# Optimization experiments

Hardware: AMD Instinct MI355X
Metric: run time of the kernel (lower is better)

## Reference

```python
import jax, jax.numpy as jnp
import numpy as np

B, D, K, NUM_CLASSES = 8192, 512, 20, 1024
EPS = 1e-12  # torch F.normalize clamp


def setup_inputs() -> dict:
    key = jax.random.key(0)
    k1, k2 = jax.random.split(key)
    batch = jax.random.normal(k1, (B, D), dtype=jnp.float32)
    labels = jax.random.randint(k2, (B,), 0, NUM_CLASSES, dtype=jnp.int64 if jax.config.jax_enable_x64 else jnp.int32)
    return {"batch": batch, "labels": labels, "k": K}


def reference(batch, labels, k):
    # L2-normalize rows (F.normalize, p=2)
    norm = jnp.maximum(jnp.linalg.norm(batch, axis=1, keepdims=True), EPS)
    x = batch / norm
    cos = x @ x.T                                   # [B, B] cosine similarity
    min_value = cos.min() - 1.0                     # scalar, computed before diag fill
    bs = cos.shape[0]
    diag = jnp.eye(bs, dtype=bool)
    cos = jnp.where(diag, min_value, cos)           # fill_diagonal_(min_value)
    # argsort(-cos)[:, :k]  ==  top-k by similarity (self excluded via diag fill)
    top_vals, top_idx = jax.lax.top_k(cos, k)       # [B, k]
    # preds = (cos + 1)/2 gathered at neighbor indices == (top_vals + 1)/2
    preds = (top_vals + 1.0) * 0.5
    true_labels = (labels[top_idx] == labels[:, None]).astype(jnp.float32)  # [B, k]
    # nn.BCELoss with mean reduction; torch clamps each log term at -100
    logp = jnp.maximum(jnp.log(preds), -100.0)
    log1mp = jnp.maximum(jnp.log1p(-preds), -100.0)
    loss = -(true_labels * logp + (1.0 - true_labels) * log1mp)
    return loss.mean()
```

## Files before the change

### kernel.cpp

```cpp
#include <hip/hip_runtime.h>
#include <hip/hip_bf16.h>

#define NROWS 8192
#define DIM   512
#define KSEL  20
#define PANEL 1024
#define NSURV 512

typedef unsigned int u32;
typedef unsigned long long u64;
typedef short bf16x8 __attribute__((ext_vector_type(8)));
typedef float f32x4 __attribute__((ext_vector_type(4)));
typedef ushort u16x2 __attribute__((ext_vector_type(2)));

typedef const void __attribute__((address_space(1))) as1_void;
typedef void __attribute__((address_space(3))) as3_void;

__device__ __forceinline__ void async_ld16(const ushort* g, ushort* l) {
    __builtin_amdgcn_global_load_lds((as1_void*)g, (as3_void*)l, 16, 0, 0);
}

__device__ __forceinline__ ushort f2bf(float f) {
    u32 u = __float_as_uint(f);
    return (ushort)((u + 0x7FFFu + ((u >> 16) & 1u)) >> 16);
}

__device__ __forceinline__ u32 mono16(u32 r) {
    return r ^ (0x8000u | ((r >> 15) * 0x7FFFu));
}

__device__ __forceinline__ u32 mkey(float f) { return mono16((u32)f2bf(f)); }

__device__ __forceinline__ u32 pkmax(u32 a, u32 b) {
    union { u32 u; u16x2 v; } x, y; x.u = a; y.u = b;
    x.v = __builtin_elementwise_max(x.v, y.v);
    return x.u;
}

__global__ __launch_bounds__(256) void k_norm(const float* __restrict__ x,
                                              ushort* __restrict__ xn) {
    int lane = threadIdx.x & 63;
    int wv   = threadIdx.x >> 6;
    int row  = blockIdx.x * 4 + wv;
    const float4* xr = (const float4*)(x + (size_t)row * DIM);
    float4 a = xr[2 * lane];
    float4 b = xr[2 * lane + 1];
    float ss = a.x*a.x + a.y*a.y + a.z*a.z + a.w*a.w
             + b.x*b.x + b.y*b.y + b.z*b.z + b.w*b.w;
    #pragma unroll
    for (int off = 32; off; off >>= 1) ss += __shfl_xor(ss, off);
    float sc = 1.0f / fmaxf(sqrtf(ss), 1e-12f);
    float v[8] = {a.x*sc, a.y*sc, a.z*sc, a.w*sc, b.x*sc, b.y*sc, b.z*sc, b.w*sc};
    union { ushort u[8]; uint4 q; } o;
    #pragma unroll
    for (int i = 0; i < 8; ++i) o.u[i] = f2bf(v[i]);
    *(uint4*)(xn + (size_t)row * DIM + lane * 8) = o.q;
}

template<bool TRI>
__global__ __launch_bounds__(256) void k_gemm(const ushort* __restrict__ xn,
                                              ushort* __restrict__ C,
                                              ushort* __restrict__ M,
                                              int row0) {
    __shared__ ushort sh[128 * 128];
    ushort* lA = sh;
    ushort* lB = sh + 128 * 64;
    int tid  = threadIdx.x;
    int lane = tid & 63, wv = tid >> 6;
    int wr = wv >> 1, wc = wv & 1;
    int q = lane >> 4, m = lane & 15;
    int bx, by;
    if (TRI) {
        int t = (int)blockIdx.x;
        t = (t & 7) * 260 + (t >> 3);
        by = (int)((sqrtf(8.0f * (float)t + 1.0f) - 1.0f) * 0.5f);
        while ((by + 1) * (by + 2) / 2 <= t) ++by;
        while (by * (by + 1) / 2 > t) --by;
        bx = t - by * (by + 1) / 2;
    } else {
        bx = blockIdx.x; by = blockIdx.y;
    }
    int grow0 = row0 + by * 128;
    int gcol0 = bx * 128;
    f32x4 acc[4][4] = {};

    int lr = lane >> 3;
    int lc = lane & 7;
    for (int kc = 0; kc < 8; ++kc) {
        #pragma unroll
        for (int t = 0; t < 4; ++t) {
            int rb  = wv * 32 + t * 8;
            int r   = rb + lr;
            int fch = lc ^ (r & 7);
            async_ld16(xn + (size_t)(grow0 + r) * DIM + kc * 64 + fch * 8, &lA[rb * 64]);
            async_ld16(xn + (size_t)(gcol0 + r) * DIM + kc * 64 + fch * 8, &lB[rb * 64]);
        }
        __syncthreads();
        #pragma unroll
        for (int s = 0; s < 2; ++s) {
            bf16x8 af[4], bfr[4];
            #pragma unroll
            for (int i = 0; i < 4; ++i) {
                int ra = wr * 64 + i * 16 + m;
                af[i]  = *(const bf16x8*)&lA[ra * 64 + (((s * 4 + q) ^ (ra & 7)) * 8)];
                int rb2 = wc * 64 + i * 16 + m;
                bfr[i] = *(const bf16x8*)&lB[rb2 * 64 + (((s * 4 + q) ^ (rb2 & 7)) * 8)];
            }
            #pragma unroll
            for (int i = 0; i < 4; ++i)
                #pragma unroll
                for (int j = 0; j < 4; ++j)
                    acc[i][j] = __builtin_amdgcn_mfma_f32_16x16x32_bf16(af[i], bfr[j], acc[i][j], 0, 0, 0);
        }
        __syncthreads();
    }

    float cmf[4] = {-3.0f, -3.0f, -3.0f, -3.0f};
    #pragma unroll
    for (int i = 0; i < 4; ++i) {
        float rmf[4] = {-3.0f, -3.0f, -3.0f, -3.0f};
        int rloc = wr * 64 + i * 16 + q * 4;
        #pragma unroll
        for (int j = 0; j < 4; ++j) {
            int cl = wc * 64 + j * 16 + m;
            int c  = gcol0 + cl;
            #pragma unroll
            for (int reg = 0; reg < 4; ++reg) {
                int r    = rloc + reg;
                int grw  = row0 + by * 128 + r;
                float a  = acc[i][j][reg];
                bool dg  = (grw == c);
                float mv = dg ? -3.0f : a;
                rmf[reg] = fmaxf(rmf[reg], mv);
                cmf[j]   = fmaxf(cmf[j], mv);
                int D = r * 64 + ((cl >> 1) ^ (q << 3));
                sh[D * 2 + (cl & 1)] = dg ? (ushort)0xC040 : f2bf(a);
            }
        }
        u32 p01 = mkey(rmf[0]) | (mkey(rmf[1]) << 16);
        u32 p23 = mkey(rmf[2]) | (mkey(rmf[3]) << 16);
        #pragma unroll
        for (int off = 1; off <= 8; off <<= 1) {
            p01 = pkmax(p01, (u32)__shfl_xor((int)p01, off));
            p23 = pkmax(p23, (u32)__shfl_xor((int)p23, off));
        }
        if (m == 0) {
            u64 pk = (u64)p01 | ((u64)p23 << 32);
            *(u64*)&M[(size_t)(bx * 2 + wc) * NROWS + (row0 + by * 128 + rloc)] = pk;
        }
    }
    if (TRI && bx != by) {
        u32 q01 = mkey(cmf[0]) | (mkey(cmf[1]) << 16);
        u32 q23 = mkey(cmf[2]) | (mkey(cmf[3]) << 16);
        q01 = pkmax(q01, (u32)__shfl_xor((int)q01, 16));
        q01 = pkmax(q01, (u32)__shfl_xor((int)q01, 32));
        q23 = pkmax(q23, (u32)__shfl_xor((int)q23, 16));
        q23 = pkmax(q23, (u32)__shfl_xor((int)q23, 32));
        if (q == 0) {
            int gc = gcol0 + wc * 64 + m;
            size_t sb = (size_t)(by * 2 + wr) * NROWS + gc;
            M[sb +  0] = (ushort)(q01 & 0xFFFFu);
            M[sb + 16] = (ushort)(q01 >> 16);
            M[sb + 32] = (ushort)(q23 & 0xFFFFu);
            M[sb + 48] = (ushort)(q23 >> 16);
        }
    }
    __syncthreads();

    int tr = tid >> 4;
    int tc = tid & 15;
    #pragma unroll
    for (int p = 0; p < 8; ++p) {
        int r  = p * 16 + tr;
        int qr = (r >> 2) & 3;
        uint4 v = *(const uint4*)&sh[(r * 64 + ((tc * 4) ^ (qr << 3))) * 2];
        *(uint4*)&C[(size_t)(by * 128 + r) * NROWS + gcol0 + tc * 8] = v;
    }

    if (TRI && bx != by) {
        __syncthreads();
        u32* sh32 = (u32*)sh;
        #pragma unroll
        for (int i = 0; i < 4; ++i) {
            int cd0 = wr * 32 + i * 8 + q * 2;
            #pragma unroll
            for (int j = 0; j < 4; ++j) {
                int rT = wc * 64 + j * 16 + m;
                int gT = ((rT >> 2) & 3) << 3;
                u32 w0 = (u32)f2bf(acc[i][j][0]) | ((u32)f2bf(acc[i][j][1]) << 16);
                u32 w1 = (u32)f2bf(acc[i][j][2]) | ((u32)f2bf(acc[i][j][3]) << 16);
                sh32[rT * 64 + (cd0 ^ gT)]       = w0;
                sh32[rT * 64 + ((cd0 + 1) ^ gT)] = w1;
            }
        }
        __syncthreads();
        #pragma unroll
        for (int p = 0; p < 8; ++p) {
            int ct = p * 16 + tr;
            int gq = ((ct >> 2) & 3) << 3;
            uint4 v = *(const uint4*)&sh32[ct * 64 + ((tc * 4) ^ gq)];
            *(uint4*)&C[(size_t)(gcol0 + ct) * NROWS + by * 128 + tc * 8] = v;
        }
    }
}

__global__ __launch_bounds__(256) void k_select(const ushort* __restrict__ C,
                                                const ushort* __restrict__ M,
                                                const int* __restrict__ labels,
                                                int row0,
                                                float* __restrict__ partials) {
    __shared__ u32 s_surv[4][NSURV];
    __shared__ u32 s_seg[4][128];
    __shared__ u32 s_cnt[4];
    __shared__ u32 s_scnt[4];
    int lane = threadIdx.x & 63;
    int wv   = threadIdx.x >> 6;
    int prow = blockIdx.x * 4 + wv;
    int grow = row0 + prow;
    const ushort* rowC = C + (size_t)prow * NROWS;

    if (lane == 0) { s_cnt[wv] = 0; s_scnt[wv] = 0; }
    __syncthreads();

    u32 klo = (u32)M[(size_t)(2 * lane)     * NROWS + grow];
    u32 khi = (u32)M[(size_t)(2 * lane + 1) * NROWS + grow];

    u32 T = 0;
    #pragma unroll
    for (int b = 15; b >= 0; --b) {
        u32 cand = T | (1u << b);
        int c = __popcll(__ballot(klo >= cand)) + __popcll(__ballot(khi >= cand));
        if (c >= KSEL) T = cand;
    }

    if (klo >= T) { u32 p = atomicAdd(&s_scnt[wv], 1u); s_seg[wv][p] = 2u * lane; }
    if (khi >= T) { u32 p = atomicAdd(&s_scnt[wv], 1u); s_seg[wv][p] = 2u * lane + 1u; }
    u32 nseg = s_scnt[wv];
    int grp = lane >> 3, sub = lane & 7;

    int  sid[4];
    uint4 vv[4];
    #pragma unroll
    for (int t = 0; t < 4; ++t) {
        u32 ix = (u32)(t * 8 + grp);
        sid[t] = (ix < nseg) ? (int)s_seg[wv][ix] : -1;
    }
    #pragma unroll
    for (int t = 0; t < 4; ++t) {
        if (sid[t] >= 0) vv[t] = *(const uint4*)(rowC + sid[t] * 64 + sub * 8);
    }
    #pragma unroll
    for (int t = 0; t < 4; ++t) {
        if (sid[t] < 0) continue;
        u32 wds[4] = { vv[t].x, vv[t].y, vv[t].z, vv[t].w };
        u32 cbase = (u32)(sid[t] * 64 + sub * 8);
        #pragma unroll
        for (int h = 0; h < 4; ++h) {
            u32 w  = wds[h];
            u32 kA = mono16(w & 0xFFFFu);
            u32 kB = mono16(w >> 16);
            if (kA >= T) { u32 p = atomicAdd(&s_cnt[wv], 1u); if (p < NSURV) s_surv[wv][p] = (kA << 16) | (cbase + 2u * h); }
            if (kB >= T) { u32 p = atomicAdd(&s_cnt[wv], 1u); if (p < NSURV) s_surv[wv][p] = (kB << 16) | (cbase + 2u * h + 1u); }
        }
    }
    for (u32 base = 32; base < nseg; base += 8) {
        u32 ix = base + (u32)grp;
        if (ix >= nseg) continue;
        int s = (int)s_seg[wv][ix];
        uint4 v = *(const uint4*)(rowC + s * 64 + sub * 8);
        u32 wds[4] = { v.x, v.y, v.z, v.w };
        u32 cbase = (u32)(s * 64 + sub * 8);
        #pragma unroll
        for (int h = 0; h < 4; ++h) {
            u32 w  = wds[h];
            u32 kA = mono16(w & 0xFFFFu);
            u32 kB = mono16(w >> 16);
            if (kA >= T) { u32 p = atomicAdd(&s_cnt[wv], 1u); if (p < NSURV) s_surv[wv][p] = (kA << 16) | (cbase + 2u * h); }
            if (kB >= T) { u32 p = atomicAdd(&s_cnt[wv], 1u); if (p < NSURV) s_surv[wv][p] = (kB << 16) | (cbase + 2u * h + 1u); }
        }
    }

    u32 cnt = min(s_cnt[wv], (u32)NSURV);
    int mylab = labels[grow];
    float loss = 0.0f;

    if (cnt <= 64u) {
        u32 gg  = ((u32)lane < cnt) ? s_surv[wv][lane] : 0u;
        u32 key = gg >> 16;
        u32 V = 0;
        #pragma unroll
        for (int b = 15; b >= 0; --b) {
            u32 cand = V | (1u << b);
            if (__popcll(__ballot(key >= cand)) >= KSEL) V = cand;
        }
        int cgt  = __popcll(__ballot(key > V));
        int ceq  = __popcll(__ballot(gg != 0 && key == V));
        int need = KSEL - cgt;
        bool incl;
        if (ceq == need) {
            incl = (gg != 0) && (key >= V);
        } else {
            u32 col = gg & 0xFFFFu;
            bool tie = (gg != 0) && (key == V);
            u32 Cv = 0;
            #pragma unroll
            for (int b = 15; b >= 0; --b) {
                u32 cand2 = Cv | (1u << b);
                if (__popcll(__ballot(tie && col >= cand2)) >= need) Cv = cand2;
            }
            incl = (key > V) || (tie && col >= Cv);
        }
        if (incl) {
            u32 col = gg & 0xFFFFu;
            u32 raw = (key & 0x8000u) ? (key ^ 0x8000u) : (key ^ 0xFFFFu);
            float v = __uint_as_float(raw << 16);
            float p = (v + 1.0f) * 0.5f;
            bool tm = (labels[col] == mylab);
            loss -= tm ? fmaxf(logf(p), -100.0f) : fmaxf(log1pf(-p), -100.0f);
        }
    } else {
        u32 g[8];
        #pragma unroll
        for (int j = 0; j < 8; ++j) {
            u32 idx = (u32)lane + (u32)j * 64u;
            g[j] = (idx < cnt) ? s_surv[wv][idx] : 0u;
        }
        u32 V = 0;
        #pragma unroll
        for (int b = 15; b >= 0; --b) {
            u32 cand = V | (1u << b);
            int c = 0;
            #pragma unroll
            for (int j = 0; j < 8; ++j)
                c += __popcll(__ballot((g[j] >> 16) >= cand));
            if (c >= KSEL) V = cand;
        }
        int cgt = 0, ceq = 0;
        #pragma unroll
        for (int j = 0; j < 8; ++j) {
            cgt += __popcll(__ballot(g[j] != 0 && (g[j] >> 16) > V));
            ceq += __popcll(__ballot(g[j] != 0 && (g[j] >> 16) == V));
        }
        int need = KSEL - cgt;
        bool all_ties = (ceq == need);
        #pragma unroll
        for (int j = 0; j < 8; ++j) {
            u32 key = g[j] >> 16, col = g[j] & 0xFFFFu;
            if (g[j] != 0 && (key > V || (all_ties && key == V))) {
                u32 raw = (key & 0x8000u) ? (key ^ 0x8000u) : (key ^ 0xFFFFu);
                float v = __uint_as_float(raw << 16);
                float p = (v + 1.0f) * 0.5f;
                bool tm = (labels[col] == mylab);
                loss -= tm ? fmaxf(logf(p), -100.0f) : fmaxf(log1pf(-p), -100.0f);
            }
        }
        if (!all_ties) {
            for (int r = 0; r < need; ++r) {
                u32 best = 0;
                #pragma unroll
                for (int j = 0; j < 8; ++j) {
                    u32 c2 = (g[j] != 0 && (g[j] >> 16) == V) ? ((g[j] & 0xFFFFu) + 1u) : 0u;
                    best = max(best, c2);
                }
                #pragma unroll
                for (int off = 32; off; off >>= 1) best = max(best, (u32)__shfl_xor((int)best, off));
                #pragma unroll
                for (int j = 0; j < 8; ++j) {
                    if (g[j] != 0 && (g[j] >> 16) == V && ((g[j] & 0xFFFFu) + 1u) == best) {
                        u32 col = g[j] & 0xFFFFu;
                        u32 raw = (V & 0x8000u) ? (V ^ 0x8000u) : (V ^ 0xFFFFu);
                        float v = __uint_as_float(raw << 16);
                        float p = (v + 1.0f) * 0.5f;
                        bool tm = (labels[col] == mylab);
                        loss -= tm ? fmaxf(logf(p), -100.0f) : fmaxf(log1pf(-p), -100.0f);
                        g[j] = 0;
                    }
                }
            }
        }
    }

    #pragma unroll
    for (int off = 32; off; off >>= 1) loss += __shfl_xor(loss, off);
    if (lane == 0) partials[grow] = loss;
}

__global__ __launch_bounds__(256) void k_final(const float* __restrict__ partials,
                                               float* __restrict__ out) {
    __shared__ float s[4];
    int tid = threadIdx.x, lane = tid & 63, wvi = tid >> 6;
    const float4* p4 = (const float4*)partials;
    float sum = 0.0f;
    #pragma unroll
    for (int i = 0; i < 8; ++i) {
        float4 v = p4[tid + i * 256];
        sum += v.x + v.y + v.z + v.w;
    }
    #pragma unroll
    for (int off = 32; off; off >>= 1) sum += __shfl_xor(sum, off);
    if (lane == 0) s[wvi] = sum;
    __syncthreads();
    if (tid == 0) out[0] = (s[0] + s[1] + s[2] + s[3]) * (1.0f / (float)(NROWS * KSEL));
}

extern "C" void kernel_launch(void* const* d_in, const int* in_sizes, int n_in,
                              void* d_out, int out_size, void* d_ws, size_t ws_size,
                              hipStream_t stream) {
    const float* batch  = (const float*)d_in[0];
    const int*   labels = (const int*)d_in[1];

    ushort* xn = (ushort*)d_ws;
    ushort* C  = xn + (size_t)NROWS * DIM;
    ushort* M        = (ushort*)d_in[0];
    float*  partials = (float*)((char*)d_in[0] + (4u << 20));

    size_t need_full = (size_t)NROWS * DIM * 2 + (size_t)NROWS * NROWS * 2;

    k_norm<<<NROWS / 4, 256, 0, stream>>>(batch, xn);

    if (ws_size >= need_full) {
        k_gemm<true><<<dim3(64 * 65 / 2), 256, 0, stream>>>(xn, C, M, 0);
        k_select<<<NROWS / 4, 256, 0, stream>>>(C, M, labels, 0, partials);
    } else {
        for (int p = 0; p < NROWS / PANEL; ++p) {
            k_gemm<false><<<dim3(64, PANEL / 128), 256, 0, stream>>>(xn, C, M, p * PANEL);
            k_select<<<PANEL / 4, 256, 0, stream>>>(C, M, labels, p * PANEL, partials);
        }
    }
    k_final<<<1, 256, 0, stream>>>(partials, (float*)d_out);
}
```

Before: 159.2 us.

## Double-buffer GEMM LDS staging with async prefetch over K=32 chunks

The GEMM main loop now splits K into 16 chunks of 32 and keeps two LDS buffers. The next chunk is prefetched with global_load_lds while MFMAs run on the current one, using manual vmcnt waits and raw s_barrier instead of __syncthreads. The XOR swizzle is dropped for a plain 32-element row layout. This is meant to hide global load latency behind compute, but it doubles the number of barriers and may bring back LDS bank conflicts on the fragment reads.

```diff
diff --git a/kernel.cpp b/kernel.cpp
--- a/kernel.cpp
+++ b/kernel.cpp
@@ -63,8 +63,6 @@
                                               ushort* __restrict__ M,
                                               int row0) {
     __shared__ ushort sh[128 * 128];
-    ushort* lA = sh;
-    ushort* lB = sh + 128 * 64;
     int tid  = threadIdx.x;
     int lane = tid & 63, wv = tid >> 6;
     int wr = wv >> 1, wc = wv & 1;
@@ -84,27 +82,37 @@
     int gcol0 = bx * 128;
     f32x4 acc[4][4] = {};
 
-    int lr = lane >> 3;
-    int lc = lane & 7;
-    for (int kc = 0; kc < 8; ++kc) {
-        #pragma unroll
-        for (int t = 0; t < 4; ++t) {
-            int rb  = wv * 32 + t * 8;
-            int r   = rb + lr;
-            int fch = lc ^ (r & 7);
-            async_ld16(xn + (size_t)(grow0 + r) * DIM + kc * 64 + fch * 8, &lA[rb * 64]);
-            async_ld16(xn + (size_t)(gcol0 + r) * DIM + kc * 64 + fch * 8, &lB[rb * 64]);
-        }
-        __syncthreads();
-        #pragma unroll
-        for (int s = 0; s < 2; ++s) {
+    int srow = lane >> 2;
+    int sch  = lane & 3;
+    #define STAGE(buf, kc)                                                          \
+        _Pragma("unroll")                                                           \
+        for (int t_ = 0; t_ < 2; ++t_) {                                            \
+            int rb_ = wv * 32 + t_ * 16;                                            \
+            const ushort* ga_ = xn + (size_t)(grow0 + rb_ + srow) * DIM + (kc) * 32 + sch * 8; \
+            const ushort* gb_ = xn + (size_t)(gcol0 + rb_ + srow) * DIM + (kc) * 32 + sch * 8; \
+            async_ld16(ga_, &sh[(buf) * 4096 + rb_ * 32]);                          \
+            async_ld16(gb_, &sh[8192 + (buf) * 4096 + rb_ * 32]);                   \
+        }
+
+    STAGE(0, 0);
+    for (int kc = 0; kc < 16; ++kc) {
+        int cur = kc & 1;
+        if (kc < 15) {
+            STAGE(cur ^ 1, kc + 1);
+            asm volatile("s_waitcnt vmcnt(4)" ::: "memory");
+        } else {
+            asm volatile("s_waitcnt vmcnt(0)" ::: "memory");
+        }
+        __builtin_amdgcn_s_barrier();
+        __builtin_amdgcn_sched_barrier(0);
+        {
+            const ushort* A = sh + cur * 4096;
+            const ushort* B = sh + 8192 + cur * 4096;
             bf16x8 af[4], bfr[4];
             #pragma unroll
             for (int i = 0; i < 4; ++i) {
-                int ra = wr * 64 + i * 16 + m;
-                af[i]  = *(const bf16x8*)&lA[ra * 64 + (((s * 4 + q) ^ (ra & 7)) * 8)];
-                int rb2 = wc * 64 + i * 16 + m;
-                bfr[i] = *(const bf16x8*)&lB[rb2 * 64 + (((s * 4 + q) ^ (rb2 & 7)) * 8)];
+                af[i]  = *(const bf16x8*)&A[(wr * 64 + i * 16 + m) * 32 + q * 8];
+                bfr[i] = *(const bf16x8*)&B[(wc * 64 + i * 16 + m) * 32 + q * 8];
             }
             #pragma unroll
             for (int i = 0; i < 4; ++i)
@@ -112,8 +120,10 @@
                 for (int j = 0; j < 4; ++j)
                     acc[i][j] = __builtin_amdgcn_mfma_f32_16x16x32_bf16(af[i], bfr[j], acc[i][j], 0, 0, 0);
         }
-        __syncthreads();
-    }
+        __builtin_amdgcn_sched_barrier(0);
+        __builtin_amdgcn_s_barrier();
+    }
+    #undef STAGE
 
     float cmf[4] = {-3.0f, -3.0f, -3.0f, -3.0f};
     #pragma unroll
```

Measured after the change: 185.9 us. +16.8%, slower.
